# Performance work log

Measured on AMD Instinct MI355X. Metric: run time of the kernel, lower is better.

The kernel has to match this reference:

```python
import jax, jax.numpy as jnp
import numpy as np

L, B, S, D = 3, 2, 2048, 1024
H, DH = 8, 128
NA, BS = 128, 16          # num_anchors, block_size
V = 32000
MASK_ID = V - 1
GAMMA = 7.0
EPS = 1e-6


def setup_inputs() -> dict:
    key = jax.random.key(0)
    ks = jax.random.split(key, 11)
    sc = 0.02
    return {
        "input_ids": jax.random.randint(ks[0], (B, S), 0, MASK_ID),
        "hidden_states": jax.random.normal(ks[1], (L, B, S, D), jnp.float32),
        "anchor_positions": jnp.sort(jax.random.randint(ks[2], (B, NA), 0, S - BS), axis=-1),
        "lm_head_weight": jax.random.normal(ks[3], (V, D), jnp.float32) * sc,
        "norm_weight": jnp.ones((D,), jnp.float32),
        "fc_weight": jax.random.normal(ks[4], (D, L * D), jnp.float32) * sc,
        "embed_table": jax.random.normal(ks[5], (V, D), jnp.float32) * sc,
        "wq": jax.random.normal(ks[6], (D, D), jnp.float32) * sc,
        "wk": jax.random.normal(ks[7], (D, D), jnp.float32) * sc,
        "wv": jax.random.normal(ks[8], (D, D), jnp.float32) * sc,
        "wo": jax.random.normal(ks[9], (D, D), jnp.float32) * sc,
    }


def _rope(x, pos):
    # x: [B, T, H, DH], pos: [B, T]
    half = DH // 2
    inv = 1.0 / (10000.0 ** (jnp.arange(half, dtype=jnp.float32) / half))
    ang = pos[..., None].astype(jnp.float32) * inv          # [B, T, half]
    cos = jnp.cos(ang)[:, :, None, :]
    sin = jnp.sin(ang)[:, :, None, :]
    x1, x2 = x[..., :half], x[..., half:]
    return jnp.concatenate([x1 * cos - x2 * sin, x1 * sin + x2 * cos], axis=-1)


def reference(input_ids, hidden_states, anchor_positions, lm_head_weight,
              norm_weight, fc_weight, embed_table, wq, wk, wv, wo):
    Q = NA * BS            # draft length
    KV = S + Q             # context + draft

    # extract_context_feature: concat target layers along feature dim, project to D
    hcat = jnp.transpose(hidden_states, (1, 2, 0, 3)).reshape(B, S, L * D)
    ctx = hcat @ fc_weight.T                                 # [B, S, D]

    # _prepare_noise_input: anchor token + (BS-1) MASK tokens per block
    offs = jnp.arange(BS)
    pos_flat = (anchor_positions[:, :, None] + offs[None, None, :]).reshape(B, Q)
    in_bounds = pos_flat < S
    gidx = jnp.minimum(pos_flat, S - 1)
    all_tokens = jnp.take_along_axis(input_ids, gidx, axis=1)  # [B, Q]
    pos_in_block = jnp.arange(Q) % BS
    is_anchor = pos_in_block == 0
    draft_ids = jnp.where(is_anchor[None, :], all_tokens, MASK_ID)
    labels = jnp.where((~is_anchor)[None, :] & in_bounds, all_tokens, -100)

    # _create_position_ids
    ctx_pid = jnp.broadcast_to(jnp.arange(S), (B, S))
    draft_pid = pos_flat                                     # block i starts at anchor_i

    # draft attention: Q from draft tokens, KV over [context_feature; draft]
    emb = embed_table[draft_ids]                             # [B, Q, D]
    q = _rope((emb @ wq.T).reshape(B, Q, H, DH), draft_pid)
    kc = _rope((ctx @ wk.T).reshape(B, S, H, DH), ctx_pid)
    kd = _rope((emb @ wk.T).reshape(B, Q, H, DH), draft_pid)
    vc = (ctx @ wv.T).reshape(B, S, H, DH)
    vd = (emb @ wv.T).reshape(B, Q, H, DH)
    k = jnp.concatenate([kc, kd], axis=1)                    # [B, KV, H, DH]
    v = jnp.concatenate([vc, vd], axis=1)

    scores = jnp.einsum('bqhd,bkhd->bhqk', q, k) / np.sqrt(DH)

    # dflash_mask_mod: block sees context before its anchor + bidirectional intra-block
    qi = jnp.arange(Q)
    kvi = jnp.arange(KV)
    qb = qi // BS                                            # [Q]
    anc = anchor_positions[:, qb]                            # [B, Q]
    ctx_vis = (kvi[None, None, :] < S) & (kvi[None, None, :] < anc[:, :, None])
    kvb = (kvi - S) // BS
    draft_vis = (kvi[None, :] >= S) & (qb[:, None] == kvb[None, :])  # [Q, KV]
    mask = ctx_vis | draft_vis[None, :, :]                   # [B, Q, KV]

    scores = jnp.where(mask[:, None, :, :], scores, jnp.float32(-1e30))
    attn = jax.nn.softmax(scores, axis=-1)
    out = jnp.einsum('bhqk,bkhd->bqhd', attn, v).reshape(B, Q, D) @ wo.T
    h = emb + out

    # final RMSNorm + frozen LM head
    h = h * jax.lax.rsqrt(jnp.mean(h * h, axis=-1, keepdims=True) + EPS) * norm_weight
    logits = h @ lm_head_weight.T                            # [B, Q, V]

    # exponential-decay-weighted cross entropy (anchor weight = 0)
    logp = jax.nn.log_softmax(logits, axis=-1)
    lbl = jnp.maximum(labels, 0)
    nll = -jnp.take_along_axis(logp, lbl[..., None], axis=-1)[..., 0]
    decay = jnp.concatenate([jnp.zeros((1,), jnp.float32),
                             jnp.exp(-(jnp.arange(1, BS, dtype=jnp.float32) - 1.0) / GAMMA)])
    w = decay[pos_in_block][None, :] * (labels != -100).astype(jnp.float32)
    loss = jnp.sum(w * nll) / jnp.maximum(jnp.sum(w), 1e-6)

    valid = labels != -100
    correct = (jnp.argmax(logits, axis=-1) == labels) & valid
    acc = jnp.sum(correct).astype(jnp.float32) / jnp.maximum(jnp.sum(valid), 1).astype(jnp.float32)
    return loss, acc
```

## Files before the change

kernel.cpp:

```cpp
#include <hip/hip_runtime.h>
#include <math.h>

typedef __attribute__((ext_vector_type(8))) short short8;
typedef __attribute__((ext_vector_type(4))) float f32x4;

#define B_ 2
#define S_ 2048
#define D_ 1024
#define H_ 8
#define DH_ 128
#define NA_ 128
#define V_ 32000
#define MASKID_ 31999
#define Q_ 2048
#define KV_ 4096
#define KVP_ 4128
#define NROWS_ 4096
#define NRC_ 3840
#define NP_ 500

__device__ __forceinline__ float bf2f(ushort u){ union{uint u;float f;}v; v.u=(uint)u<<16; return v.f; }
__device__ __forceinline__ ushort f2bf(float f){ union{float f;uint u;}v; v.f=f; return (ushort)((v.u + 0x7fffu + ((v.u>>16)&1u))>>16); }

__device__ __forceinline__ f32x4 mfma16(short8 a, short8 b, f32x4 c){
  return __builtin_amdgcn_mfma_f32_16x16x32_bf16(a,b,c,0,0,0);
}
__device__ __forceinline__ float rmax16(float v){
  #pragma unroll
  for(int m=1;m<16;m<<=1) v = fmaxf(v, __shfl_xor(v,m));
  return v;
}
__device__ __forceinline__ float rsum16(float v){
  #pragma unroll
  for(int m=1;m<16;m<<=1) v += __shfl_xor(v,m);
  return v;
}

__global__ void k_meta(const int* __restrict__ ids, const int* __restrict__ anch,
                       int* __restrict__ draft, int* __restrict__ lab2, int* __restrict__ posf){
  int idx = blockIdx.x*256 + threadIdx.x;
  if (idx >= NROWS_) return;
  int b = idx >> 11, i = idx & (Q_-1);
  int p = i & 15;
  int a = anch[b*NA_ + (i>>4)];
  int pos = a + p;
  posf[idx] = pos;
  int gi = pos < S_ ? pos : S_-1;
  int tok = ids[b*S_ + gi];
  bool isa = (p==0);
  draft[idx] = isa ? tok : MASKID_;
  if (!isa){
    int rc = (idx >> 4)*15 + (p - 1);
    lab2[rc] = tok;
  }
}

__global__ void k_prep(const float* __restrict__ hs,
    const float* __restrict__ fcw, const float* __restrict__ wq, const float* __restrict__ wk,
    const float* __restrict__ wv, const float* __restrict__ wo, const float* __restrict__ lmw,
    const float* __restrict__ et, const int* __restrict__ ids, const int* __restrict__ anch,
    ushort* __restrict__ hc, ushort* __restrict__ fcW, ushort* __restrict__ Wqkv,
    ushort* __restrict__ woW, ushort* __restrict__ lmW, ushort* __restrict__ emb){
  int idx = blockIdx.x*256 + threadIdx.x;
  const float* src; ushort* dst; size_t so, doff;
  if (idx < 1572864){
    int f8 = idx % 384; int row = idx / 384;
    int b = row >> 11, s = row & (S_-1);
    int f0 = f8*8, l = f0 >> 10, d = f0 & 1023;
    src = hs; so = (((size_t)l*B_ + b)*S_ + s)*D_ + d;
    dst = hc; doff = (size_t)row*3072 + f0;
  } else if (idx < 6586368){
    int i = idx - 1572864;
    int j;
    if (i < 393216){ src = fcw; dst = fcW; j = i; }
    else if (i < 524288){ src = wq;  dst = Wqkv;                    j = i - 393216; }
    else if (i < 655360){ src = wk;  dst = Wqkv + (size_t)1048576;  j = i - 524288; }
    else if (i < 786432){ src = wv;  dst = Wqkv + (size_t)2097152;  j = i - 655360; }
    else if (i < 917504){ src = wo;  dst = woW;                     j = i - 786432; }
    else               { src = lmw; dst = lmW;                     j = i - 917504; }
    so = (size_t)j*8; doff = (size_t)j*8;
  } else if (idx < 7110656){
    int j = idx - 6586368;
    int row = j >> 7, c = (j & 127)*8;
    int b = row >> 11, i = row & (Q_-1);
    int p = i & 15;
    int a = anch[b*NA_ + (i>>4)];
    int pos = a + p;
    int gi = pos < S_ ? pos : S_-1;
    int tok = ids[b*S_ + gi];
    int id = (p==0) ? tok : MASKID_;
    src = et; so = (size_t)id*D_ + c;
    dst = emb; doff = (size_t)row*D_ + c;
  } else return;
  const float4* s4 = (const float4*)(src + so);
  float4 a = s4[0], b = s4[1];
  short8 u;
  u[0]=(short)f2bf(a.x); u[1]=(short)f2bf(a.y); u[2]=(short)f2bf(a.z); u[3]=(short)f2bf(a.w);
  u[4]=(short)f2bf(b.x); u[5]=(short)f2bf(b.y); u[6]=(short)f2bf(b.z); u[7]=(short)f2bf(b.w);
  *(short8*)(dst + doff) = u;
}

__device__ __forceinline__ void gemm_body(const ushort* __restrict__ A, const ushort* __restrict__ Bm,
    void* __restrict__ C, int N, int K, int bm, int bn, int OBF, ushort* lA, ushort* lB){
  const int lane = threadIdx.x & 63, w = threadIdx.x >> 6;
  const int l15 = lane & 15, g = lane >> 4;
  const int wm = w >> 1, wn = w & 1;
  f32x4 acc[4][4];
  #pragma unroll
  for (int a0=0;a0<4;++a0)
    #pragma unroll
    for (int a1=0;a1<4;++a1) acc[a0][a1] = f32x4{0.f,0.f,0.f,0.f};
  int rowS[2], kgS[2];
  #pragma unroll
  for (int i=0;i<2;++i){
    int o = w*1024 + i*4096 + lane*16;
    rowS[i] = o >> 6;
    kgS[i] = (((o>>4)&3) - (rowS[i]>>1)) & 3;
  }
  for (int k0 = 0; k0 < K; k0 += 32){
    #pragma unroll
    for (int i=0;i<2;++i){
      const ushort* sa = A + (size_t)(bm*128 + rowS[i])*K + k0 + kgS[i]*8;
      const ushort* sb = Bm + (size_t)(bn*128 + rowS[i])*K + k0 + kgS[i]*8;
      __builtin_amdgcn_global_load_lds((const __attribute__((address_space(1))) void*)sa,
          (__attribute__((address_space(3))) void*)((char*)lA + w*1024 + i*4096), 16, 0, 0);
      __builtin_amdgcn_global_load_lds((const __attribute__((address_space(1))) void*)sb,
          (__attribute__((address_space(3))) void*)((char*)lB + w*1024 + i*4096), 16, 0, 0);
    }
    __syncthreads();
    short8 af[4], bf[4];
    #pragma unroll
    for (int mf=0;mf<4;++mf){
      int rr = wm*64 + mf*16 + l15;
      af[mf] = *(const short8*)((const char*)lA + rr*64 + (((g + (rr>>1))&3)*16));
    }
    #pragma unroll
    for (int nf=0;nf<4;++nf){
      int rr = wn*64 + nf*16 + l15;
      bf[nf] = *(const short8*)((const char*)lB + rr*64 + (((g + (rr>>1))&3)*16));
    }
    #pragma unroll
    for (int mf=0;mf<4;++mf)
      #pragma unroll
      for (int nf=0;nf<4;++nf)
        acc[mf][nf] = mfma16(af[mf], bf[nf], acc[mf][nf]);
    __syncthreads();
  }
  #pragma unroll
  for (int mf=0;mf<4;++mf)
  #pragma unroll
  for (int nf=0;nf<4;++nf){
    int row0 = bm*128 + wm*64 + mf*16 + g*4;
    int col  = bn*128 + wn*64 + nf*16 + l15;
    #pragma unroll
    for (int r=0;r<4;++r){
      if (OBF) ((ushort*)C)[(size_t)(row0+r)*N + col] = f2bf(acc[mf][nf][r]);
      else     ((float*)C)[(size_t)(row0+r)*N + col] = acc[mf][nf][r];
    }
  }
}

template<int OBF>
__global__ __launch_bounds__(256) void k_gemm(const ushort* __restrict__ A, const ushort* __restrict__ Bm,
                       void* __restrict__ C, int N, int K){
  __shared__ ushort lA[128*32];
  __shared__ ushort lB[128*32];
  gemm_body(A, Bm, C, N, K, blockIdx.x, blockIdx.y, OBF, lA, lB);
}

__global__ __launch_bounds__(256) void k_fcqkv(const ushort* __restrict__ hcat, const ushort* __restrict__ fcW,
    ushort* __restrict__ ctx, const ushort* __restrict__ emb, const ushort* __restrict__ Wqkv,
    ushort* __restrict__ C1){
  __shared__ ushort lA[128*32];
  __shared__ ushort lB[128*32];
  int bid = blockIdx.x;
  if (bid < 256){
    gemm_body(hcat, fcW, ctx, 1024, 3072, bid & 31, bid >> 5, 1, lA, lB);
  } else {
    int t = bid - 256;
    gemm_body(emb, Wqkv, C1, 3072, 1024, t & 31, t >> 5, 1, lA, lB);
  }
}

__global__ __launch_bounds__(256) void k_lmgemm(const ushort* __restrict__ A, const ushort* __restrict__ Bm,
    float* __restrict__ pm, float* __restrict__ pl, int* __restrict__ pbi){
  __shared__ ushort lA[128*32];
  __shared__ ushort lB[128*32];
  const int bm = blockIdx.x, bn = blockIdx.y;
  if (bm >= 30) return;
  const int lane = threadIdx.x & 63, w = threadIdx.x >> 6;
  const int l15 = lane & 15, g = lane >> 4;
  const int wm = w >> 1, wn = w & 1;
  f32x4 acc[4][4];
  #pragma unroll
  for (int a0=0;a0<4;++a0)
    #pragma unroll
    for (int a1=0;a1<4;++a1) acc[a0][a1] = f32x4{0.f,0.f,0.f,0.f};
  int rowS[2], kgS[2];
  #pragma unroll
  for (int i=0;i<2;++i){
    int o = w*1024 + i*4096 + lane*16;
    rowS[i] = o >> 6;
    kgS[i] = (((o>>4)&3) - (rowS[i]>>1)) & 3;
  }
  for (int k0 = 0; k0 < 1024; k0 += 32){
    #pragma unroll
    for (int i=0;i<2;++i){
      const ushort* sa = A + (size_t)(bm*128 + rowS[i])*1024 + k0 + kgS[i]*8;
      const ushort* sb = Bm + (size_t)(bn*128 + rowS[i])*1024 + k0 + kgS[i]*8;
      __builtin_amdgcn_global_load_lds((const __attribute__((address_space(1))) void*)sa,
          (__attribute__((address_space(3))) void*)((char*)lA + w*1024 + i*4096), 16, 0, 0);
      __builtin_amdgcn_global_load_lds((const __attribute__((address_space(1))) void*)sb,
          (__attribute__((address_space(3))) void*)((char*)lB + w*1024 + i*4096), 16, 0, 0);
    }
    __syncthreads();
    short8 af[4], bfr[4];
    #pragma unroll
    for (int mf=0;mf<4;++mf){
      int rr = wm*64 + mf*16 + l15;
      af[mf] = *(const short8*)((const char*)lA + rr*64 + (((g + (rr>>1))&3)*16));
    }
    #pragma unroll
    for (int nf=0;nf<4;++nf){
      int rr = wn*64 + nf*16 + l15;
      bfr[nf] = *(const short8*)((const char*)lB + rr*64 + (((g + (rr>>1))&3)*16));
    }
    #pragma unroll
    for (int mf=0;mf<4;++mf)
      #pragma unroll
      for (int nf=0;nf<4;++nf)
        acc[mf][nf] = mfma16(af[mf], bfr[nf], acc[mf][nf]);
    __syncthreads();
  }
  const int colb = bn*128 + wn*64 + l15;
  #pragma unroll
  for (int mf=0;mf<4;++mf){
    #pragma unroll
    for (int r=0;r<4;++r){
      float s0 = acc[mf][0][r], s1 = acc[mf][1][r], s2 = acc[mf][2][r], s3 = acc[mf][3][r];
      float M = rmax16(fmaxf(fmaxf(s0,s1), fmaxf(s2,s3)));
      float lsum = rsum16(__expf(s0-M) + __expf(s1-M) + __expf(s2-M) + __expf(s3-M));
      int ci = 0x7fffffff;
      if (s3 == M) ci = colb+48;
      if (s2 == M) ci = colb+32;
      if (s1 == M) ci = colb+16;
      if (s0 == M) ci = colb;
      #pragma unroll
      for (int msk=1; msk<16; msk<<=1){
        int oi = __shfl_xor(ci, msk);
        ci = oi < ci ? oi : ci;
      }
      if (l15 == 0){
        int row = bm*128 + wm*64 + mf*16 + g*4 + r;
        size_t pidx = (size_t)(bn*2 + wn)*NRC_ + row;
        pm[pidx] = M; pl[pidx] = lsum; pbi[pidx] = ci;
      }
    }
  }
}

__global__ __launch_bounds__(256) void k_lbl(const ushort* __restrict__ hb, const float* __restrict__ wv,
    const int* __restrict__ lab2, float* __restrict__ plbl){
  const int lane = threadIdx.x & 63, w = threadIdx.x >> 6;
  const int row = blockIdx.x*4 + w;
  int lab = lab2[row];
  const ushort* hr = hb + (size_t)row*1024 + lane*16;
  const float* wr = wv + (size_t)lab*1024 + lane*16;
  short8 h0 = *(const short8*)hr, h1 = *(const short8*)(hr+8);
  float4 w0 = *(const float4*)wr, w1 = *(const float4*)(wr+4);
  float4 w2 = *(const float4*)(wr+8), w3 = *(const float4*)(wr+12);
  float s = 0.f;
  s += bf2f((ushort)h0[0])*w0.x + bf2f((ushort)h0[1])*w0.y + bf2f((ushort)h0[2])*w0.z + bf2f((ushort)h0[3])*w0.w;
  s += bf2f((ushort)h0[4])*w1.x + bf2f((ushort)h0[5])*w1.y + bf2f((ushort)h0[6])*w1.z + bf2f((ushort)h0[7])*w1.w;
  s += bf2f((ushort)h1[0])*w2.x + bf2f((ushort)h1[1])*w2.y + bf2f((ushort)h1[2])*w2.z + bf2f((ushort)h1[3])*w2.w;
  s += bf2f((ushort)h1[4])*w3.x + bf2f((ushort)h1[5])*w3.y + bf2f((ushort)h1[6])*w3.z + bf2f((ushort)h1[7])*w3.w;
  #pragma unroll
  for (int msk=1; msk<64; msk<<=1) s += __shfl_xor(s, msk);
  if (lane == 0) plbl[row] = s;
}

__global__ void k_ropeall(const ushort* __restrict__ C1, const ushort* __restrict__ C2,
    const int* __restrict__ posf, ushort* __restrict__ qb, ushort* __restrict__ kb,
    ushort* __restrict__ vT){
  int idx = blockIdx.x*256 + threadIdx.x;
  if (idx < 2097152){
    int d2 = idx & 63, h = (idx>>6)&7, i = (idx>>9)&(Q_-1), b = idx>>20;
    int row = b*Q_ + i;
    int pos = posf[row];
    float inv = __expf(-(float)d2 * 0.14391156831212787f);
    float ang = (float)pos * inv;
    float sn, cs; __sincosf(ang, &sn, &cs);
    const ushort* cr = C1 + (size_t)row*3072 + h*DH_ + d2;
    float x1 = bf2f(cr[0]), x2 = bf2f(cr[64]);
    size_t qo = (size_t)row*D_ + h*DH_ + d2;
    qb[qo] = f2bf(x1*cs - x2*sn); qb[qo+64] = f2bf(x1*sn + x2*cs);
    x1 = bf2f(cr[1024]); x2 = bf2f(cr[1088]);
    size_t ko = ((size_t)(b*KV_ + S_ + i))*D_ + h*DH_ + d2;
    kb[ko] = f2bf(x1*cs - x2*sn); kb[ko+64] = f2bf(x1*sn + x2*cs);
    x1 = bf2f(cr[2048]); x2 = bf2f(cr[2112]);
    size_t vo = ((size_t)((b*H_ + h)*DH_ + d2))*KVP_ + (S_ + i);
    vT[vo] = f2bf(x1); vT[vo + (size_t)64*KVP_] = f2bf(x2);
  } else if (idx < 4194304){
    int t = idx - 2097152;
    int d2 = t & 63, h = (t>>6)&7, i = (t>>9)&(S_-1), b = t>>20;
    int row = b*S_ + i;
    float inv = __expf(-(float)d2 * 0.14391156831212787f);
    float ang = (float)i * inv;
    float sn, cs; __sincosf(ang, &sn, &cs);
    const ushort* cr = C2 + (size_t)row*2048 + h*DH_ + d2;
    float x1 = bf2f(cr[0]), x2 = bf2f(cr[64]);
    size_t ko = ((size_t)(b*KV_ + i))*D_ + h*DH_ + d2;
    kb[ko] = f2bf(x1*cs - x2*sn); kb[ko+64] = f2bf(x1*sn + x2*cs);
    x1 = bf2f(cr[1024]); x2 = bf2f(cr[1088]);
    size_t vo = ((size_t)((b*H_ + h)*DH_ + d2))*KVP_ + i;
    vT[vo] = f2bf(x1); vT[vo + (size_t)64*KVP_] = f2bf(x2);
  } else if (idx < 4259840){
    int t = idx - 4194304;
    int row = t >> 5, c = t & 31;
    vT[(size_t)row*KVP_ + 4096 + c] = 0;
  }
}

__global__ __launch_bounds__(512) void k_attn(const ushort* __restrict__ qb, const ushort* __restrict__ kb,
    const ushort* __restrict__ vT, const int* __restrict__ anch, ushort* __restrict__ ao){
  __shared__ ushort pbuf[8][16*72];
  __shared__ float mrg[4][16][128];
  __shared__ float mml[4][2][16];
  const int lane = threadIdx.x & 63, w = threadIdx.x >> 6;
  const int l15 = lane & 15, g = lane >> 4;
  const int wt = w & 3, half = w >> 2;
  const int gi = blockIdx.x;
  const int logical = (gi & 7)*64 + (gi >> 3);
  const int b = logical >> 8, h = (logical >> 5) & 7;
  const int qblk = (logical & 31)*4 + wt;
  const int anc = anch[b*NA_ + qblk];
  ushort* pb = pbuf[w];
  short8 aq[4];
  {
    const ushort* qr = qb + ((size_t)(b*Q_ + qblk*16 + l15))*D_ + h*DH_ + g*8;
    #pragma unroll
    for (int kc=0;kc<4;++kc) aq[kc] = *(const short8*)(qr + kc*32);
  }
  f32x4 o[8];
  #pragma unroll
  for (int cc=0;cc<8;++cc) o[cc] = f32x4{0.f,0.f,0.f,0.f};
  float m[4] = {-1e30f,-1e30f,-1e30f,-1e30f};
  float sl[4] = {0.f,0.f,0.f,0.f};
  const float SC = 0.08838834764831845f;
  const ushort* vbase = vT + ((size_t)((b*H_ + h)*DH_))*KVP_;

  auto process = [&](int kv0, int limit){
    const int nk = limit - kv0;
    f32x4 sc[4];
    #pragma unroll
    for (int f=0;f<4;++f) sc[f] = f32x4{0.f,0.f,0.f,0.f};
    const ushort* kr = kb + ((size_t)(b*KV_ + kv0 + l15))*D_ + h*DH_ + g*8;
    #pragma unroll
    for (int f=0;f<4;++f){
      if (f*16 < nk){
        const ushort* krf = kr + (size_t)(f*16)*D_;
        #pragma unroll
        for (int kc=0;kc<4;++kc){
          short8 bk = *(const short8*)(krf + kc*32);
          sc[f] = mfma16(aq[kc], bk, sc[f]);
        }
      }
    }
    #pragma unroll
    for (int r=0;r<4;++r){
      float s0 = (kv0 + l15      < limit) ? sc[0][r]*SC : -1e30f;
      float s1 = (kv0 + 16 + l15 < limit) ? sc[1][r]*SC : -1e30f;
      float s2 = (kv0 + 32 + l15 < limit) ? sc[2][r]*SC : -1e30f;
      float s3 = (kv0 + 48 + l15 < limit) ? sc[3][r]*SC : -1e30f;
      float cm = rmax16(fmaxf(fmaxf(s0,s1), fmaxf(s2,s3)));
      float mn = fmaxf(m[r], cm);
      float esc = __expf(m[r] - mn);
      float p0 = __expf(s0 - mn), p1 = __expf(s1 - mn);
      float p2 = __expf(s2 - mn), p3 = __expf(s3 - mn);
      float rs = rsum16(p0 + p1 + p2 + p3);
      sl[r] = sl[r]*esc + rs;
      m[r] = mn;
      #pragma unroll
      for (int cc=0;cc<8;++cc) o[cc][r] *= esc;
      int q = g*4 + r;
      pb[q*72 + l15]      = f2bf(p0);
      pb[q*72 + 16 + l15] = f2bf(p1);
      pb[q*72 + 32 + l15] = f2bf(p2);
      pb[q*72 + 48 + l15] = f2bf(p3);
    }
    asm volatile("s_waitcnt lgkmcnt(0)" ::: "memory");
    __builtin_amdgcn_sched_barrier(0);
    const ushort* pr = pb + l15*72 + g*8;
    short8 pa0 = *(const short8*)pr;
    const ushort* vr = vbase + kv0 + g*8;
    #pragma unroll
    for (int cc=0;cc<8;++cc){
      short8 bv = *(const short8*)(vr + (size_t)(cc*16 + l15)*KVP_);
      o[cc] = mfma16(pa0, bv, o[cc]);
    }
    if (nk > 32){
      short8 pa1 = *(const short8*)(pr + 32);
      const ushort* vr2 = vr + 32;
      #pragma unroll
      for (int cc=0;cc<8;++cc){
        short8 bv = *(const short8*)(vr2 + (size_t)(cc*16 + l15)*KVP_);
        o[cc] = mfma16(pa1, bv, o[cc]);
      }
    }
  };
  for (int kv0 = half*64; kv0 < anc; kv0 += 128) process(kv0, anc);
  if (half == 1){
    int kv0 = S_ + qblk*16;
    process(kv0, kv0 + 16);
    #pragma unroll
    for (int cc=0;cc<8;++cc)
      #pragma unroll
      for (int r=0;r<4;++r)
        mrg[wt][g*4+r][cc*16+l15] = o[cc][r];
    if (l15 == 0){
      #pragma unroll
      for (int r=0;r<4;++r){ mml[wt][0][g*4+r] = m[r]; mml[wt][1][g*4+r] = sl[r]; }
    }
  }
  __syncthreads();
  if (half == 0){
    #pragma unroll
    for (int r=0;r<4;++r){
      float m1 = mml[wt][0][g*4+r], l1 = mml[wt][1][g*4+r];
      float mn = fmaxf(m[r], m1);
      float e0 = __expf(m[r] - mn), e1 = __expf(m1 - mn);
      float lm = sl[r]*e0 + l1*e1;
      int q = g*4 + r;
      #pragma unroll
      for (int cc=0;cc<8;++cc){
        float val = (o[cc][r]*e0 + mrg[wt][q][cc*16+l15]*e1) / lm;
        ao[((size_t)(b*Q_ + qblk*16 + q))*D_ + h*DH_ + cc*16 + l15] = f2bf(val);
      }
    }
  }
}

__global__ __launch_bounds__(256) void k_rms(const float* __restrict__ wo_out, const float* __restrict__ et,
    const int* __restrict__ draft, const float* __restrict__ nw, ushort* __restrict__ hb){
  const int rc = blockIdx.x, tid = threadIdx.x;
  const int row = (rc/15)*16 + rc%15 + 1;
  const int lane = tid & 63, w = tid >> 6;
  const float* wr = wo_out + (size_t)row*D_;
  const float* er = et + (size_t)draft[row]*D_;
  float v[4]; float ss = 0.f;
  #pragma unroll
  for (int j=0;j<4;++j){
    int d = tid + j*256;
    v[j] = er[d] + wr[d];
    ss += v[j]*v[j];
  }
  #pragma unroll
  for (int msk=1; msk<64; msk<<=1) ss += __shfl_xor(ss, msk);
  __shared__ float red[4];
  if (lane == 0) red[w] = ss;
  __syncthreads();
  float tot = red[0]+red[1]+red[2]+red[3];
  float rs = rsqrtf(tot*(1.f/1024.f) + 1e-6f);
  #pragma unroll
  for (int j=0;j<4;++j){
    int d = tid + j*256;
    hb[(size_t)rc*D_ + d] = f2bf(v[j]*rs*nw[d]);
  }
}

__global__ __launch_bounds__(256) void k_combine(const float* __restrict__ pm, const float* __restrict__ pl,
    const int* __restrict__ pbi, const float* __restrict__ plbl,
    const int* __restrict__ lab2, float* __restrict__ pblk){
  const int lane = threadIdx.x & 63, w = threadIdx.x >> 6;
  const int row = blockIdx.x*4 + w;
  float M = -1e30f, Lx = 0.f;
  float bv = -1e30f; int bi = 0x7fffffff;
  for (int s = lane; s < NP_; s += 64){
    size_t idx = (size_t)s*NRC_ + row;
    float mm = pm[idx], ll = pl[idx];
    float Mn = fmaxf(M, mm);
    Lx = Lx*__expf(M-Mn) + ll*__expf(mm-Mn);
    M = Mn;
    int ii = pbi[idx];
    if (mm > bv || (mm == bv && ii < bi)){ bv = mm; bi = ii; }
  }
  #pragma unroll
  for (int msk=1; msk<64; msk<<=1){
    float Mo = __shfl_xor(M, msk), Lo = __shfl_xor(Lx, msk);
    float bvo = __shfl_xor(bv, msk); int bio = __shfl_xor(bi, msk);
    float Mn = fmaxf(M, Mo);
    Lx = Lx*__expf(M-Mn) + Lo*__expf(Mo-Mn);
    M = Mn;
    if (bvo > bv || (bvo == bv && bio < bi)){ bv = bvo; bi = bio; }
  }
  __shared__ float red[4][4];
  if (lane == 0){
    float logZ = M + logf(Lx);
    float lb = plbl[row];
    int lab = lab2[row];
    float wgt = __expf(-(float)(row%15)*(1.f/7.f));
    float nll = logZ - lb;
    red[w][0] = wgt*nll;
    red[w][1] = wgt;
    red[w][2] = (bi == lab) ? 1.f : 0.f;
    red[w][3] = 1.f;
  }
  __syncthreads();
  if (threadIdx.x == 0){
    float s0=0,s1=0,s2=0,s3=0;
    for (int i=0;i<4;++i){ s0+=red[i][0]; s1+=red[i][1]; s2+=red[i][2]; s3+=red[i][3]; }
    pblk[blockIdx.x*4+0]=s0; pblk[blockIdx.x*4+1]=s1; pblk[blockIdx.x*4+2]=s2; pblk[blockIdx.x*4+3]=s3;
  }
}

__global__ void k_final(const float* __restrict__ pblk, float* __restrict__ out){
  const int t = threadIdx.x;
  float s0=0,s1=0,s2=0,s3=0;
  for (int i=t; i<960; i+=256){
    const float4 v = *(const float4*)(pblk + i*4);
    s0+=v.x; s1+=v.y; s2+=v.z; s3+=v.w;
  }
  #pragma unroll
  for (int msk=1; msk<64; msk<<=1){
    s0+=__shfl_xor(s0,msk); s1+=__shfl_xor(s1,msk);
    s2+=__shfl_xor(s2,msk); s3+=__shfl_xor(s3,msk);
  }
  __shared__ float red[4][4];
  int lane = t & 63, w = t >> 6;
  if (lane==0){ red[w][0]=s0; red[w][1]=s1; red[w][2]=s2; red[w][3]=s3; }
  __syncthreads();
  if (t==0){
    float a0=red[0][0]+red[1][0]+red[2][0]+red[3][0];
    float a1=red[0][1]+red[1][1]+red[2][1]+red[3][1];
    float a2=red[0][2]+red[1][2]+red[2][2]+red[3][2];
    float a3=red[0][3]+red[1][3]+red[2][3]+red[3][3];
    out[0]=a0/fmaxf(a1,1e-6f);
    out[1]=a2/fmaxf(a3,1.f);
  }
}

extern "C" void kernel_launch(void* const* d_in, const int* in_sizes, int n_in,
                              void* d_out, int out_size, void* d_ws, size_t ws_size,
                              hipStream_t stream){
  const int*   ids  = (const int*)d_in[0];
  const float* hs   = (const float*)d_in[1];
  const int*   anch = (const int*)d_in[2];
  const float* lmw  = (const float*)d_in[3];
  const float* nw   = (const float*)d_in[4];
  const float* fcw  = (const float*)d_in[5];
  const float* et   = (const float*)d_in[6];
  const float* wq   = (const float*)d_in[7];
  const float* wk   = (const float*)d_in[8];
  const float* wvp  = (const float*)d_in[9];
  const float* wo   = (const float*)d_in[10];
  float* out = (float*)d_out;
  (void)in_sizes; (void)n_in; (void)out_size; (void)ws_size;

  char* ws = (char*)d_ws;
  size_t off = 0;
  auto alloc = [&](size_t bytes)->char*{ char* p = ws + off; off = (off + bytes + 255) & ~(size_t)255; return p; };
  ushort* fcW   = (ushort*)alloc((size_t)1024*3072*2);
  ushort* Wqkv  = (ushort*)alloc((size_t)3072*1024*2);
  ushort* woW   = (ushort*)alloc((size_t)1024*1024*2);
  ushort* lmW   = (ushort*)alloc((size_t)V_*1024*2);
  ushort* ctx   = (ushort*)alloc((size_t)4096*1024*2);
  ushort* emb   = (ushort*)alloc((size_t)4096*1024*2);
  ushort* hcat  = (ushort*)alloc((size_t)4096*3072*2);
  ushort* C1 = hcat;
  ushort* C2    = (ushort*)alloc((size_t)4096*2048*2);
  float* wo_out = (float*)C2;
  ushort* qbuf  = (ushort*)alloc((size_t)4096*1024*2);
  ushort* kbuf  = (ushort*)alloc((size_t)B_*KV_*1024*2);
  ushort* vT    = (ushort*)alloc((size_t)B_*H_*DH_*KVP_*2);
  ushort* ao    = (ushort*)alloc((size_t)4096*1024*2);
  ushort* hb    = (ushort*)alloc((size_t)NRC_*1024*2);
  int* draft  = (int*)alloc(4096*4);
  int* lab2   = (int*)alloc(NRC_*4);
  int* posf   = (int*)alloc(4096*4);
  float* plbl = (float*)alloc(NRC_*4);
  float* pblk = (float*)alloc(960*4*4);
  float* pm  = (float*)ctx;
  float* pl  = (float*)emb;
  int*   pbi = (int*)hcat;

  k_meta<<<16,256,0,stream>>>(ids, anch, draft, lab2, posf);
  k_prep<<<27776,256,0,stream>>>(hs, fcw, wq, wk, wvp, wo, lmw, et, ids, anch,
                                 hcat, fcW, Wqkv, woW, lmW, emb);
  k_fcqkv<<<1024,256,0,stream>>>(hcat, fcW, ctx, emb, Wqkv, C1);
  k_gemm<1><<<dim3(32,16),256,0,stream>>>(ctx, Wqkv + (size_t)1024*1024, C2, 2048, 1024);
  k_ropeall<<<16640,256,0,stream>>>(C1, C2, posf, qbuf, kbuf, vT);
  k_attn<<<512,512,0,stream>>>(qbuf, kbuf, vT, anch, ao);
  k_gemm<0><<<dim3(32,8),256,0,stream>>>(ao, woW, wo_out, 1024, 1024);
  k_rms<<<NRC_,256,0,stream>>>(wo_out, et, draft, nw, hb);
  k_lbl<<<960,256,0,stream>>>(hb, lmw, lab2, plbl);
  k_lmgemm<<<dim3(32,250),256,0,stream>>>(hb, lmW, pm, pl, pbi);
  k_combine<<<960,256,0,stream>>>(pm, pl, pbi, plbl, lab2, pblk);
  k_final<<<1,256,0,stream>>>(pblk, out);
}
```

Before: 798.4 us.

## Double LM-head GEMM K-tile and fuse label logit dot into RMSNorm

The LM-head GEMM now stages a 64-wide K slice per iteration as two 32-wide LDS planes, halving the number of barrier pairs and load rounds over the K loop. The separate label-logit kernel is removed and its dot product is computed inside the RMSNorm kernel on the fp32 normalized values, saving one launch and a reread of hb. LDS use per block doubles, which may reduce occupancy. The label logit now uses fp32 rather than bf16-rounded activations, a slight numeric change.

```diff
diff --git a/kernel.cpp b/kernel.cpp
--- a/kernel.cpp
+++ b/kernel.cpp
@@ -184,8 +184,8 @@
 
 __global__ __launch_bounds__(256) void k_lmgemm(const ushort* __restrict__ A, const ushort* __restrict__ Bm,
     float* __restrict__ pm, float* __restrict__ pl, int* __restrict__ pbi){
-  __shared__ ushort lA[128*32];
-  __shared__ ushort lB[128*32];
+  __shared__ ushort lA[128*64];
+  __shared__ ushort lB[128*64];
   const int bm = blockIdx.x, bn = blockIdx.y;
   if (bm >= 30) return;
   const int lane = threadIdx.x & 63, w = threadIdx.x >> 6;
@@ -196,40 +196,47 @@
   for (int a0=0;a0<4;++a0)
     #pragma unroll
     for (int a1=0;a1<4;++a1) acc[a0][a1] = f32x4{0.f,0.f,0.f,0.f};
-  int rowS[2], kgS[2];
-  #pragma unroll
-  for (int i=0;i<2;++i){
+  int srcO[4];
+  #pragma unroll
+  for (int i=0;i<4;++i){
     int o = w*1024 + i*4096 + lane*16;
-    rowS[i] = o >> 6;
-    kgS[i] = (((o>>4)&3) - (rowS[i]>>1)) & 3;
-  }
-  for (int k0 = 0; k0 < 1024; k0 += 32){
-    #pragma unroll
-    for (int i=0;i<2;++i){
-      const ushort* sa = A + (size_t)(bm*128 + rowS[i])*1024 + k0 + kgS[i]*8;
-      const ushort* sb = Bm + (size_t)(bn*128 + rowS[i])*1024 + k0 + kgS[i]*8;
-      __builtin_amdgcn_global_load_lds((const __attribute__((address_space(1))) void*)sa,
+    int p = o >> 13, o2 = o & 8191;
+    int r = o2 >> 6;
+    int kg = (((o2>>4)&3) - (r>>1)) & 3;
+    srcO[i] = r*1024 + p*32 + kg*8;
+  }
+  const ushort* Ab = A + (size_t)bm*128*1024;
+  const ushort* Bb = Bm + (size_t)bn*128*1024;
+  for (int k0 = 0; k0 < 1024; k0 += 64){
+    #pragma unroll
+    for (int i=0;i<4;++i){
+      __builtin_amdgcn_global_load_lds((const __attribute__((address_space(1))) void*)(Ab + k0 + srcO[i]),
           (__attribute__((address_space(3))) void*)((char*)lA + w*1024 + i*4096), 16, 0, 0);
-      __builtin_amdgcn_global_load_lds((const __attribute__((address_space(1))) void*)sb,
+      __builtin_amdgcn_global_load_lds((const __attribute__((address_space(1))) void*)(Bb + k0 + srcO[i]),
           (__attribute__((address_space(3))) void*)((char*)lB + w*1024 + i*4096), 16, 0, 0);
     }
     __syncthreads();
-    short8 af[4], bfr[4];
-    #pragma unroll
-    for (int mf=0;mf<4;++mf){
-      int rr = wm*64 + mf*16 + l15;
-      af[mf] = *(const short8*)((const char*)lA + rr*64 + (((g + (rr>>1))&3)*16));
-    }
-    #pragma unroll
-    for (int nf=0;nf<4;++nf){
-      int rr = wn*64 + nf*16 + l15;
-      bfr[nf] = *(const short8*)((const char*)lB + rr*64 + (((g + (rr>>1))&3)*16));
-    }
-    #pragma unroll
-    for (int mf=0;mf<4;++mf)
-      #pragma unroll
-      for (int nf=0;nf<4;++nf)
-        acc[mf][nf] = mfma16(af[mf], bfr[nf], acc[mf][nf]);
+    #pragma unroll
+    for (int pl2=0; pl2<2; ++pl2){
+      const char* bA = (const char*)lA + pl2*8192;
+      const char* bB = (const char*)lB + pl2*8192;
+      short8 af[4], bfr[4];
+      #pragma unroll
+      for (int mf=0;mf<4;++mf){
+        int rr = wm*64 + mf*16 + l15;
+        af[mf] = *(const short8*)(bA + rr*64 + (((g + (rr>>1))&3)*16));
+      }
+      #pragma unroll
+      for (int nf=0;nf<4;++nf){
+        int rr = wn*64 + nf*16 + l15;
+        bfr[nf] = *(const short8*)(bB + rr*64 + (((g + (rr>>1))&3)*16));
+      }
+      #pragma unroll
+      for (int mf=0;mf<4;++mf)
+        #pragma unroll
+        for (int nf=0;nf<4;++nf)
+          acc[mf][nf] = mfma16(af[mf], bfr[nf], acc[mf][nf]);
+    }
     __syncthreads();
   }
   const int colb = bn*128 + wn*64 + l15;
@@ -257,26 +264,6 @@
       }
     }
   }
-}
-
-__global__ __launch_bounds__(256) void k_lbl(const ushort* __restrict__ hb, const float* __restrict__ wv,
-    const int* __restrict__ lab2, float* __restrict__ plbl){
-  const int lane = threadIdx.x & 63, w = threadIdx.x >> 6;
-  const int row = blockIdx.x*4 + w;
-  int lab = lab2[row];
-  const ushort* hr = hb + (size_t)row*1024 + lane*16;
-  const float* wr = wv + (size_t)lab*1024 + lane*16;
-  short8 h0 = *(const short8*)hr, h1 = *(const short8*)(hr+8);
-  float4 w0 = *(const float4*)wr, w1 = *(const float4*)(wr+4);
-  float4 w2 = *(const float4*)(wr+8), w3 = *(const float4*)(wr+12);
-  float s = 0.f;
-  s += bf2f((ushort)h0[0])*w0.x + bf2f((ushort)h0[1])*w0.y + bf2f((ushort)h0[2])*w0.z + bf2f((ushort)h0[3])*w0.w;
-  s += bf2f((ushort)h0[4])*w1.x + bf2f((ushort)h0[5])*w1.y + bf2f((ushort)h0[6])*w1.z + bf2f((ushort)h0[7])*w1.w;
-  s += bf2f((ushort)h1[0])*w2.x + bf2f((ushort)h1[1])*w2.y + bf2f((ushort)h1[2])*w2.z + bf2f((ushort)h1[3])*w2.w;
-  s += bf2f((ushort)h1[4])*w3.x + bf2f((ushort)h1[5])*w3.y + bf2f((ushort)h1[6])*w3.z + bf2f((ushort)h1[7])*w3.w;
-  #pragma unroll
-  for (int msk=1; msk<64; msk<<=1) s += __shfl_xor(s, msk);
-  if (lane == 0) plbl[row] = s;
 }
 
 __global__ void k_ropeall(const ushort* __restrict__ C1, const ushort* __restrict__ C2,
@@ -441,7 +428,8 @@
 }
 
 __global__ __launch_bounds__(256) void k_rms(const float* __restrict__ wo_out, const float* __restrict__ et,
-    const int* __restrict__ draft, const float* __restrict__ nw, ushort* __restrict__ hb){
+    const int* __restrict__ draft, const float* __restrict__ nw, const int* __restrict__ lab2,
+    const float* __restrict__ lmw, ushort* __restrict__ hb, float* __restrict__ plbl){
   const int rc = blockIdx.x, tid = threadIdx.x;
   const int row = (rc/15)*16 + rc%15 + 1;
   const int lane = tid & 63, w = tid >> 6;
@@ -457,15 +445,25 @@
   #pragma unroll
   for (int msk=1; msk<64; msk<<=1) ss += __shfl_xor(ss, msk);
   __shared__ float red[4];
+  __shared__ float red2[4];
   if (lane == 0) red[w] = ss;
   __syncthreads();
   float tot = red[0]+red[1]+red[2]+red[3];
   float rs = rsqrtf(tot*(1.f/1024.f) + 1e-6f);
+  const float* lr = lmw + (size_t)lab2[rc]*D_;
+  float sdot = 0.f;
   #pragma unroll
   for (int j=0;j<4;++j){
     int d = tid + j*256;
-    hb[(size_t)rc*D_ + d] = f2bf(v[j]*rs*nw[d]);
-  }
+    float x = v[j]*rs*nw[d];
+    hb[(size_t)rc*D_ + d] = f2bf(x);
+    sdot += x * lr[d];
+  }
+  #pragma unroll
+  for (int msk=1; msk<64; msk<<=1) sdot += __shfl_xor(sdot, msk);
+  if (lane == 0) red2[w] = sdot;
+  __syncthreads();
+  if (tid == 0) plbl[rc] = red2[0]+red2[1]+red2[2]+red2[3];
 }
 
 __global__ __launch_bounds__(256) void k_combine(const float* __restrict__ pm, const float* __restrict__ pl,
@@ -591,8 +589,7 @@
   k_ropeall<<<16640,256,0,stream>>>(C1, C2, posf, qbuf, kbuf, vT);
   k_attn<<<512,512,0,stream>>>(qbuf, kbuf, vT, anch, ao);
   k_gemm<0><<<dim3(32,8),256,0,stream>>>(ao, woW, wo_out, 1024, 1024);
-  k_rms<<<NRC_,256,0,stream>>>(wo_out, et, draft, nw, hb);
-  k_lbl<<<960,256,0,stream>>>(hb, lmw, lab2, plbl);
+  k_rms<<<NRC_,256,0,stream>>>(wo_out, et, draft, nw, lab2, lmw, hb, plbl);
   k_lmgemm<<<dim3(32,250),256,0,stream>>>(hb, lmW, pm, pl, pbi);
   k_combine<<<960,256,0,stream>>>(pm, pl, pbi, plbl, lab2, pblk);
   k_final<<<1,256,0,stream>>>(pblk, out);
```

After: 877.8 us. 9.9% more time.
